# Kernel optimization log

Hardware: AMD Instinct MI355X
Metric: run time of the kernel (lower is better)

The kernel has to match this reference:

```python
import jax, jax.numpy as jnp
import numpy as np

B, S, DIM, H, FR = 2, 1568, 768, 12, 8  # S = FR * 196 spatial tokens, head_dim = 64


def setup_inputs() -> dict:
    key = jax.random.key(0)
    ks = jax.random.split(key, 8)
    s = 0.02
    return {
        "xq": jax.random.normal(ks[0], (B, S, DIM), jnp.float32),
        "xk": jax.random.normal(ks[1], (B, S, DIM), jnp.float32),
        "Wq": jax.random.normal(ks[2], (DIM, DIM), jnp.float32) * s,
        "Wkv": jax.random.normal(ks[3], (DIM, 2 * DIM), jnp.float32) * s,
        "Wpq": jax.random.normal(ks[4], (DIM, DIM), jnp.float32) * s,
        "Wpkv": jax.random.normal(ks[5], (DIM, 2 * DIM), jnp.float32) * s,
        "Wproj": jax.random.normal(ks[6], (DIM, DIM), jnp.float32) * s,
        "bproj": jnp.zeros((DIM,), jnp.float32),
        "num_frames": FR,
    }


def reference(xq, xk, Wq, Wkv, Wpq, Wpkv, Wproj, bproj, num_frames):
    b, s, dim = xq.shape
    f = num_frames
    n = xk.shape[1] // f          # spatial tokens per frame
    h = H
    d = dim // h
    scale = d ** -0.5

    # stage 1: space attention per frame
    q = (xq @ Wq).reshape(b, s, h, d).transpose(0, 2, 1, 3)            # b h s d
    k, v = jnp.split(xk @ Wkv, 2, axis=-1)
    k = k.reshape(b, f * n, h, d).transpose(0, 2, 1, 3)                # b h m d
    v = v.reshape(b, f * n, h, d).transpose(0, 2, 1, 3)                # b h m d
    qk = jnp.einsum('bhsd,bhmd->bhsm', q, k).reshape(b, h, s, f, n)
    attn = jax.nn.softmax(scale * qk, axis=-1)                         # b h s f n
    vf = v.reshape(b, h, f, n, d)
    x = jnp.einsum('bhsfn,bhfnd->bhsfd', attn, vf)                     # b h s f d
    x = x.transpose(0, 2, 3, 1, 4).reshape(b, s, f, dim)               # b s f (h d)

    # diagonal gather: trajectory token for its own frame
    xg = x.reshape(b, f, n, f, dim)
    x_diag = jnp.diagonal(xg, axis1=1, axis2=3)                        # b n dim f
    x_diag = x_diag.transpose(0, 3, 1, 2).reshape(b, s, dim)           # b (f n) dim

    # stage 2: temporal attention over frames
    q2 = (x_diag @ Wpq).reshape(b, s, h, d).transpose(0, 2, 1, 3) * scale  # b h s d
    k2, v2 = jnp.split(x @ Wpkv, 2, axis=-1)
    k2 = k2.reshape(b, s, f, h, d).transpose(0, 3, 1, 2, 4)            # b h s f d
    v2 = v2.reshape(b, s, f, h, d).transpose(0, 3, 1, 2, 4)
    attn2 = jax.nn.softmax(jnp.einsum('bhsd,bhsfd->bhsf', q2, k2), axis=-1)
    out = jnp.einsum('bhsf,bhsfd->bhsd', attn2, v2)                    # b h s d
    out = out.transpose(0, 2, 1, 3).reshape(b, s, dim) @ Wproj + bproj
    return (out, attn2)
```

## Files before the change

### kernel.cpp

```cpp
#include <hip/hip_runtime.h>

#define BDIM 2
#define SEQ  1568
#define DIM  768
#define NH   12
#define FR   8
#define NTOK 196
#define HD   64
#define MTOT (BDIM*SEQ)
#define M2   (MTOT*FR)

typedef __attribute__((ext_vector_type(8))) short s16x8;
typedef __attribute__((ext_vector_type(4))) float f32x4;
typedef __attribute__((ext_vector_type(16))) float f32x16;
typedef __attribute__((ext_vector_type(4))) int i32x4;

static __device__ __forceinline__ float bf2f(ushort u) {
  return __uint_as_float(((unsigned)u) << 16);
}
static __device__ __forceinline__ ushort f2bf(float f) {
  unsigned u = __float_as_uint(f);
  unsigned r = (u + 0x7fffu + ((u >> 16) & 1u)) >> 16;
  return (ushort)r;
}
static __device__ __forceinline__ f32x4 mfma16(s16x8 a, s16x8 b, f32x4 c) {
  return __builtin_amdgcn_mfma_f32_16x16x32_bf16(a, b, c, 0, 0, 0);
}
static __device__ __forceinline__ f32x16 mfma32(s16x8 a, s16x8 b, f32x16 c) {
  return __builtin_amdgcn_mfma_f32_32x32x16_bf16(a, b, c, 0, 0, 0);
}
static __device__ __forceinline__ int cvtpk(float lo, float hi) {
  int r;
  asm("v_cvt_pk_bf16_f32 %0, %1, %2" : "=v"(r) : "v"(lo), "v"(hi));
  return r;
}
static __device__ __forceinline__ void gload_lds16(const ushort* g, ushort* l) {
  __builtin_amdgcn_global_load_lds(
      (const __attribute__((address_space(1))) void*)g,
      (__attribute__((address_space(3))) void*)l, 16, 0, 0);
}

__global__ __launch_bounds__(256)
void cvt_all(const float* __restrict__ xq, const float* __restrict__ xk,
             ushort* __restrict__ xqbf, ushort* __restrict__ xkbf,
             const float* __restrict__ Wq, const float* __restrict__ Wkv,
             const float* __restrict__ Wpq, const float* __restrict__ Wproj,
             const float* __restrict__ Wpkv,
             ushort* __restrict__ WqT, ushort* __restrict__ WkvT,
             ushort* __restrict__ WpqT, ushort* __restrict__ WprT,
             ushort* __restrict__ Wpk_bf, ushort* __restrict__ Wpv_bf,
             int n4) {
  __shared__ float T[64][65];
  const int blk = blockIdx.x;
  const int tid = threadIdx.x;

  if (blk < 4704) {
    int i = blk*256 + tid;
    const float* src; ushort* dst; int j;
    if (i < n4)        { src = xq; dst = xqbf; j = i; }
    else               { src = xk; dst = xkbf; j = i - n4; }
    float4 v = ((const float4*)src)[j];
    ushort4 o; o.x = f2bf(v.x); o.y = f2bf(v.y); o.z = f2bf(v.z); o.w = f2bf(v.w);
    ((ushort4*)dst)[j] = o;
    return;
  }

  if (blk < 5856) {
    int idx = blk - 4704;
    const int wid = idx / 288; idx %= 288;
    const int ky = idx / 24;
    const int nx = idx % 24;
    const float* W; ushort* WT; int N;
    switch (wid) {
      case 0: W = Wq;    WT = WqT;   N = DIM;   break;
      case 1: W = Wkv;   WT = WkvT;  N = 2*DIM; break;
      case 2: W = Wpq;   WT = WpqT;  N = DIM;   break;
      default: W = Wproj; WT = WprT; N = DIM;   break;
    }
    if (nx >= N/64) return;
    #pragma unroll
    for (int it = 0; it < 4; it++) {
      int id2 = it*256 + tid;
      int r = id2 >> 4, c4 = (id2 & 15) << 2;
      float4 v = *(const float4*)&W[(size_t)(ky*64 + r)*N + nx*64 + c4];
      T[r][c4+0] = v.x; T[r][c4+1] = v.y; T[r][c4+2] = v.z; T[r][c4+3] = v.w;
    }
    __syncthreads();
    #pragma unroll
    for (int it = 0; it < 4; it++) {
      int id2 = it*256 + tid;
      int n = id2 >> 4, k4 = (id2 & 15) << 2;
      ushort4 o;
      o.x = f2bf(T[k4+0][n]); o.y = f2bf(T[k4+1][n]);
      o.z = f2bf(T[k4+2][n]); o.w = f2bf(T[k4+3][n]);
      *(ushort4*)&WT[(size_t)(nx*64 + n)*DIM + ky*64 + k4] = o;
    }
    return;
  }

  {
    int id2 = blk - 5856;
    int half = id2 / 576;
    int e = (id2 % 576)*256 + tid;
    int r = e / 192;
    int c4 = (e % 192) * 4;
    float4 v = *(const float4*)&Wpkv[(size_t)r*(2*DIM) + half*DIM + c4];
    ushort4 o; o.x = f2bf(v.x); o.y = f2bf(v.y); o.z = f2bf(v.z); o.w = f2bf(v.w);
    ushort* dst = half ? Wpv_bf : Wpk_bf;
    *(ushort4*)&dst[(size_t)r*DIM + c4] = o;
  }
}

__global__ __launch_bounds__(256)
void vtrans(const ushort* __restrict__ kvbf, ushort* __restrict__ Vt) {
  __shared__ ushort Vl[NTOK][72];
  const int x = blockIdx.x;
  const int h = x % NH, f = (x / NH) % FR, b = x / (NH*FR);
  const int tid = threadIdx.x;
  for (int idx = tid; idx < NTOK*16; idx += 256) {
    int n = idx >> 4, c4 = (idx & 15) << 2;
    const ushort* p = kvbf + (size_t)(b*SEQ + f*NTOK + n)*(2*DIM) + DIM + h*HD + c4;
    *(ushort4*)&Vl[n][c4] = *(const ushort4*)p;
  }
  __syncthreads();
  ushort* vb = Vt + (size_t)x * (HD*224);
  for (int idx = tid; idx < 64*56; idx += 256) {
    int d = idx / 56, n4 = (idx % 56) << 2;
    ushort4 o;
    o.x = (n4+0 < NTOK) ? Vl[n4+0][d] : (ushort)0;
    o.y = (n4+1 < NTOK) ? Vl[n4+1][d] : (ushort)0;
    o.z = (n4+2 < NTOK) ? Vl[n4+2][d] : (ushort)0;
    o.w = (n4+3 < NTOK) ? Vl[n4+3][d] : (ushort)0;
    *(ushort4*)&vb[(size_t)d*224 + n4] = o;
  }
}

__global__ __launch_bounds__(256)
void proj_pair(const ushort* __restrict__ xqbf, const ushort* __restrict__ xkbf,
               const ushort* __restrict__ WqT, const ushort* __restrict__ WkvT,
               ushort* __restrict__ qbf, ushort* __restrict__ kvbf)
{
  __shared__ ushort As[128][32];
  __shared__ ushort Bs[64][32];
  const int bx = blockIdx.x, by = blockIdx.y;
  const ushort* A; const ushort* Bt; ushort* C; int N, col0; float scale;
  if (bx < 12) { A = xqbf; Bt = WqT;  C = qbf;  N = DIM;   col0 = bx*64;      scale = 0.125f; }
  else         { A = xkbf; Bt = WkvT; C = kvbf; N = 2*DIM; col0 = (bx-12)*64; scale = 1.0f; }

  const int tid = threadIdx.x;
  const int w = tid >> 6, lane = tid & 63;
  const int lq = lane & 15, quad = lane >> 4;
  const int lrow = tid >> 2, lcol = (tid & 3) << 3;

  int ar0 = by*128 + lrow;       if (ar0 > MTOT-1) ar0 = MTOT-1;
  int ar1 = by*128 + 64 + lrow;  if (ar1 > MTOT-1) ar1 = MTOT-1;
  const size_t aoff0 = (size_t)ar0*DIM + lcol;
  const size_t aoff1 = (size_t)ar1*DIM + lcol;
  const size_t boff  = (size_t)(col0 + lrow)*DIM + lcol;

  f32x4 acc[2][4] = {};
  for (int k0 = 0; k0 < DIM; k0 += 32) {
    __syncthreads();
    gload_lds16(A  + aoff0 + k0, &As[w*16][0]);
    gload_lds16(A  + aoff1 + k0, &As[64 + w*16][0]);
    gload_lds16(Bt + boff  + k0, &Bs[w*16][0]);
    __syncthreads();
    s16x8 af[2], bw[4];
    #pragma unroll
    for (int i = 0; i < 2; i++) af[i] = *(const s16x8*)&As[w*32 + i*16 + lq][quad*8];
    #pragma unroll
    for (int j = 0; j < 4; j++) bw[j] = *(const s16x8*)&Bs[j*16 + lq][quad*8];
    #pragma unroll
    for (int i = 0; i < 2; i++)
      #pragma unroll
      for (int j = 0; j < 4; j++)
        acc[i][j] = mfma16(af[i], bw[j], acc[i][j]);
  }

  #pragma unroll
  for (int i = 0; i < 2; i++) {
    #pragma unroll
    for (int r = 0; r < 4; r++) {
      int row = by*128 + w*32 + i*16 + quad*4 + r;
      if (row < MTOT) {
        #pragma unroll
        for (int j = 0; j < 4; j++)
          C[(size_t)row*N + col0 + j*16 + lq] = f2bf(acc[i][j][r] * scale);
      }
    }
  }
}

template<bool BIAS, bool DIAG, bool BF16OUT>
__global__ __launch_bounds__(256)
void gemm64(const ushort* __restrict__ A, const ushort* __restrict__ Bt,
            void* __restrict__ Cv, const float* __restrict__ bias,
            int M, int N, float scale)
{
  __shared__ ushort As[128][32];
  __shared__ ushort Bs[64][32];
  const int bx = blockIdx.x, by = blockIdx.y;
  const int tid = threadIdx.x;
  const int w = tid >> 6, lane = tid & 63;
  const int lq = lane & 15, quad = lane >> 4;
  const int lrow = tid >> 2, lcol = (tid & 3) << 3;
  const int col0 = bx*64;

  int ar0 = by*128 + lrow;       if (ar0 > M-1) ar0 = M-1;
  int ar1 = by*128 + 64 + lrow;  if (ar1 > M-1) ar1 = M-1;
  size_t aoff0, aoff1;
  if (DIAG) {
    int f0 = (ar0 % SEQ) / NTOK, f1 = (ar1 % SEQ) / NTOK;
    aoff0 = ((size_t)ar0*FR + f0)*DIM + lcol;
    aoff1 = ((size_t)ar1*FR + f1)*DIM + lcol;
  } else {
    aoff0 = (size_t)ar0*DIM + lcol;
    aoff1 = (size_t)ar1*DIM + lcol;
  }
  const size_t boff = (size_t)(col0 + lrow)*DIM + lcol;

  f32x4 acc[2][4] = {};
  for (int k0 = 0; k0 < DIM; k0 += 32) {
    __syncthreads();
    gload_lds16(A  + aoff0 + k0, &As[w*16][0]);
    gload_lds16(A  + aoff1 + k0, &As[64 + w*16][0]);
    gload_lds16(Bt + boff  + k0, &Bs[w*16][0]);
    __syncthreads();
    s16x8 af[2], bw[4];
    #pragma unroll
    for (int i = 0; i < 2; i++) af[i] = *(const s16x8*)&As[w*32 + i*16 + lq][quad*8];
    #pragma unroll
    for (int j = 0; j < 4; j++) bw[j] = *(const s16x8*)&Bs[j*16 + lq][quad*8];
    #pragma unroll
    for (int i = 0; i < 2; i++)
      #pragma unroll
      for (int j = 0; j < 4; j++)
        acc[i][j] = mfma16(af[i], bw[j], acc[i][j]);
  }

  #pragma unroll
  for (int i = 0; i < 2; i++) {
    #pragma unroll
    for (int r = 0; r < 4; r++) {
      int row = by*128 + w*32 + i*16 + quad*4 + r;
      if (row < M) {
        #pragma unroll
        for (int j = 0; j < 4; j++) {
          int col = col0 + j*16 + lq;
          float v = acc[i][j][r] * scale;
          if (BIAS) v += bias[col];
          if (BF16OUT) ((ushort*)Cv)[(size_t)row*N + col] = f2bf(v);
          else         ((float*)Cv)[(size_t)row*N + col] = v;
        }
      }
    }
  }
}

__global__ __launch_bounds__(256)
void qwgemm(const ushort* __restrict__ q2bf, const ushort* __restrict__ Wpk,
            ushort* __restrict__ qw)
{
  __shared__ ushort As[128][32];
  __shared__ ushort Bs[64][32];
  const int bx = blockIdx.x, by = blockIdx.y;
  const int h = bx / 12, cb = bx % 12;
  const int tid = threadIdx.x;
  const int w = tid >> 6, lane = tid & 63;
  const int lq = lane & 15, quad = lane >> 4;
  const int lrow = tid >> 2, lcol = (tid & 3) << 3;

  int ar0 = by*128 + lrow;       if (ar0 > MTOT-1) ar0 = MTOT-1;
  int ar1 = by*128 + 64 + lrow;  if (ar1 > MTOT-1) ar1 = MTOT-1;
  const size_t aoff0 = (size_t)ar0*DIM + h*HD + lcol;
  const size_t aoff1 = (size_t)ar1*DIM + h*HD + lcol;
  const size_t boff  = (size_t)(cb*64 + lrow)*DIM + h*HD + lcol;

  f32x4 acc[2][4] = {};
  #pragma unroll
  for (int k0 = 0; k0 < 64; k0 += 32) {
    __syncthreads();
    gload_lds16(q2bf + aoff0 + k0, &As[w*16][0]);
    gload_lds16(q2bf + aoff1 + k0, &As[64 + w*16][0]);
    gload_lds16(Wpk  + boff  + k0, &Bs[w*16][0]);
    __syncthreads();
    s16x8 af[2], bw[4];
    #pragma unroll
    for (int i = 0; i < 2; i++) af[i] = *(const s16x8*)&As[w*32 + i*16 + lq][quad*8];
    #pragma unroll
    for (int jj = 0; jj < 4; jj++) bw[jj] = *(const s16x8*)&Bs[jj*16 + lq][quad*8];
    #pragma unroll
    for (int i = 0; i < 2; i++)
      #pragma unroll
      for (int jj = 0; jj < 4; jj++)
        acc[i][jj] = mfma16(af[i], bw[jj], acc[i][jj]);
  }

  #pragma unroll
  for (int i = 0; i < 2; i++) {
    #pragma unroll
    for (int r = 0; r < 4; r++) {
      int row = by*128 + w*32 + i*16 + quad*4 + r;
      if (row < MTOT) {
        #pragma unroll
        for (int jj = 0; jj < 4; jj++) {
          int cl = cb*64 + jj*16 + lq;
          qw[(size_t)row*(NH*DIM) + h*DIM + cl] = f2bf(acc[i][r == r ? i*0 + jj : jj][r]);
        }
      }
    }
  }
}

__global__ __launch_bounds__(256)
void logits_sa(const ushort* __restrict__ qw, const ushort* __restrict__ x,
               float* __restrict__ attn2, ushort* __restrict__ xa)
{
  __shared__ ushort xs[4*8*792];
  __shared__ ushort qws[4*12*792];
  __shared__ float  a_s[4][NH][FR];
  const int tid = threadIdx.x;
  const int t0 = blockIdx.x * 4;

  #pragma unroll
  for (int r = 0; r < 12; ++r) {
    int id = r*256 + tid;
    int tf = id / 96, v8 = id % 96;
    int ch = v8 >> 5, cc = v8 & 31;
    s16x8 v = *(const s16x8*)(x + ((size_t)(t0 + (tf >> 3))*FR + (tf & 7))*DIM + v8*8);
    *(s16x8*)&xs[tf*792 + ch*264 + cc*8] = v;
  }
  #pragma unroll
  for (int r = 0; r < 18; ++r) {
    int id = r*256 + tid;
    int th = id / 96, v8 = id % 96;
    int ch = v8 >> 5, cc = v8 & 31;
    s16x8 v = *(const s16x8*)(qw + (size_t)(t0 + th/12)*(NH*DIM) + (th%12)*DIM + v8*8);
    *(s16x8*)&qws[th*792 + ch*264 + cc*8] = v;
  }
  __syncthreads();

  const int w = tid >> 6, lane = tid & 63;
  const int lq = lane & 15, quad = lane >> 4;
  const int fr = lq & 7;
  const int hc = (lq < 12) ? lq : 0;
  f32x4 acc = {};
  #pragma unroll
  for (int ks = 0; ks < 24; ++ks) {
    int ch = ks >> 3, cc = (ks & 7) * 32;
    s16x8 a = *(const s16x8*)&xs[(w*8 + fr)*792 + ch*264 + cc + quad*8];
    s16x8 b = *(const s16x8*)&qws[(w*12 + hc)*792 + ch*264 + cc + quad*8];
    acc = mfma16(a, b, acc);
  }

  float m4 = fmaxf(fmaxf(acc[0], acc[1]), fmaxf(acc[2], acc[3]));
  float M = fmaxf(m4, __shfl_xor(m4, 16));
  float e0 = __expf(acc[0]-M), e1 = __expf(acc[1]-M);
  float e2 = __expf(acc[2]-M), e3 = __expf(acc[3]-M);
  float s4 = (e0+e1)+(e2+e3);
  float S = s4 + __shfl_xor(s4, 16);
  float inv = 1.0f / S;
  if (quad < 2 && lq < 12) {
    int gt = t0 + w;
    int b = gt / SEQ, sI = gt % SEQ;
    float4 av; av.x = e0*inv; av.y = e1*inv; av.z = e2*inv; av.w = e3*inv;
    *(float4*)(attn2 + ((size_t)(b*NH + hc)*SEQ + sI)*FR + quad*4) = av;
    a_s[w][hc][quad*4+0] = av.x; a_s[w][hc][quad*4+1] = av.y;
    a_s[w][hc][quad*4+2] = av.z; a_s[w][hc][quad*4+3] = av.w;
  }
  __syncthreads();

  #pragma unroll
  for (int it = 0; it < 2; ++it) {
    int id = it*256 + tid;
    if (id < 384) {
      int tt = id / 96, v8 = id % 96;
      int ch = v8 >> 5, cc = v8 & 31;
      int h = v8 >> 3;
      float av[8] = {};
      #pragma unroll
      for (int f = 0; f < FR; ++f) {
        float a = a_s[tt][h][f];
        s16x8 xv = *(const s16x8*)&xs[(tt*8 + f)*792 + ch*264 + cc*8];
        #pragma unroll
        for (int e = 0; e < 8; ++e) av[e] += a * bf2f((ushort)xv[e]);
      }
      ushort4 o0, o1;
      o0.x = f2bf(av[0]); o0.y = f2bf(av[1]); o0.z = f2bf(av[2]); o0.w = f2bf(av[3]);
      o1.x = f2bf(av[4]); o1.y = f2bf(av[5]); o1.z = f2bf(av[6]); o1.w = f2bf(av[7]);
      ushort* op = xa + (size_t)(t0 + tt)*DIM + v8*8;
      *(ushort4*)op = o0; *(ushort4*)(op + 4) = o1;
    }
  }
}

__global__ __launch_bounds__(256)
void stage1_mfma(const ushort* __restrict__ qbf, const ushort* __restrict__ kvbf,
                 const ushort* __restrict__ Vt, ushort* __restrict__ x)
{
  __shared__ ushort sh[208*64];

  const int bh = blockIdx.x;
  const int f  = blockIdx.y;
  const int qt = blockIdx.z;
  const int b = bh / NH, h = bh % NH;
  const int tid = threadIdx.x;
  const int w = tid >> 6, lane = tid & 63;
  const int l31 = lane & 31, hl = lane >> 5;

  const ushort* kbase = kvbf + ((size_t)b*SEQ + f*NTOK)*(2*DIM) + h*HD;
  #pragma unroll
  for (int p = 0; p < 6; ++p) {
    const int c = w*6 + p;
    const int row = c*8 + (lane >> 3);
    const ushort* src = kbase + (size_t)row*(2*DIM)
                      + (((lane & 7) ^ (lane >> 3)) << 3);
    gload_lds16(src, &sh[c*512]);
  }
  {
    const int row = 192 + (tid >> 4);
    const int c4  = (tid & 15) << 2;
    ushort4 v; v.x = 0; v.y = 0; v.z = 0; v.w = 0;
    if (row < NTOK)
      v = *(const ushort4*)(kbase + (size_t)row*(2*DIM) + c4);
    *(ushort4*)&sh[row*64 + ((((c4 >> 3) ^ (row & 7)) << 3) | (c4 & 7))] = v;
  }

  int qrow = qt*128 + w*32 + l31; if (qrow > SEQ-1) qrow = SEQ-1;
  const ushort* qp = qbf + ((size_t)b*SEQ + qrow)*DIM + h*HD + hl*8;
  const s16x8 bq0 = *(const s16x8*)(qp);
  const s16x8 bq1 = *(const s16x8*)(qp + 16);
  const s16x8 bq2 = *(const s16x8*)(qp + 32);
  const s16x8 bq3 = *(const s16x8*)(qp + 48);

  __syncthreads();

  f32x16 acc[7];
  {
    f32x16 z = {};
    #pragma unroll
    for (int nt = 0; nt < 7; ++nt) acc[nt] = z;
  }
  const int sx = l31 & 7;
  #pragma unroll
  for (int nt = 0; nt < 7; ++nt) {
    const int rl = (nt == 6) ? (l31 & 15) : l31;
    const int rbase = (nt*32 + rl)*64;
    acc[nt] = mfma32(*(const s16x8*)&sh[rbase + (((0 + hl) ^ sx) << 3)], bq0, acc[nt]);
    acc[nt] = mfma32(*(const s16x8*)&sh[rbase + (((2 + hl) ^ sx) << 3)], bq1, acc[nt]);
    acc[nt] = mfma32(*(const s16x8*)&sh[rbase + (((4 + hl) ^ sx) << 3)], bq2, acc[nt]);
    acc[nt] = mfma32(*(const s16x8*)&sh[rbase + (((6 + hl) ^ sx) << 3)], bq3, acc[nt]);
  }

  __syncthreads();

  float s0 = 0.f, s1 = 0.f, s2 = 0.f, s3 = 0.f;
  #pragma unroll
  for (int nt = 0; nt < 7; ++nt) {
    #pragma unroll
    for (int g = 0; g < 16; ++g) {
      float e;
      if (nt == 6) {
        if (g < 4) { e = __expf(acc[6][g]); if (hl) e = 0.f; }
        else e = 0.f;
      } else {
        e = __expf(acc[nt][g]);
      }
      acc[nt][g] = e;
      if ((g & 3) == 0) s0 += e; else if ((g & 3) == 1) s1 += e;
      else if ((g & 3) == 2) s2 += e; else s3 += e;
    }
  }
  float sum = (s0 + s1) + (s2 + s3);
  sum += __shfl_xor(sum, 32);
  const float sinv = 1.0f / sum;

  f32x16 o0, o1;
  { f32x16 z = {}; o0 = z; o1 = z; }
  const ushort* vb = Vt + ((size_t)((b*FR + f)*NH + h)) * (HD*224);
  const ushort* vr0 = vb + (size_t)l31*224 + hl*8;
  const ushort* vr1 = vr0 + 32*224;
  #pragma unroll
  for (int nt = 0; nt < 7; ++nt) {
    #pragma unroll
    for (int kh = 0; kh < 2; ++kh) {
      int w0 = cvtpk(acc[nt][8*kh+0], acc[nt][8*kh+1]);
      int w1 = cvtpk(acc[nt][8*kh+2], acc[nt][8*kh+3]);
      int w2 = cvtpk(acc[nt][8*kh+4], acc[nt][8*kh+5]);
      int w3 = cvtpk(acc[nt][8*kh+6], acc[nt][8*kh+7]);
      asm("v_permlane32_swap_b32 %0, %1" : "+v"(w0), "+v"(w2));
      asm("v_permlane32_swap_b32 %0, %1" : "+v"(w1), "+v"(w3));
      union { i32x4 i; s16x8 s; } u;
      u.i.x = w0; u.i.y = w1; u.i.z = w2; u.i.w = w3;
      const int ks = nt*2 + kh;
      const s16x8 va0 = *(const s16x8*)(vr0 + ks*16);
      const s16x8 va1 = *(const s16x8*)(vr1 + ks*16);
      o0 = mfma32(va0, u.s, o0);
      o1 = mfma32(va1, u.s, o1);
    }
  }

  ushort* XT = sh + w*2048;
  #pragma unroll
  for (int dt = 0; dt < 2; ++dt) {
    #pragma unroll
    for (int c = 0; c < 4; ++c) {
      #pragma unroll
      for (int rp = 0; rp < 2; ++rp) {
        const float lo = (dt ? o1[4*c + 2*rp]     : o0[4*c + 2*rp])     * sinv;
        const float hi = (dt ? o1[4*c + 2*rp + 1] : o0[4*c + 2*rp + 1]) * sinv;
        const int word = cvtpk(lo, hi);
        const int d = dt*32 + 8*c + 4*hl + 2*rp;
        *(uint*)&XT[l31*64 + (((d >> 3) ^ (l31 & 7)) << 3) + (d & 7)] = (uint)word;
      }
    }
  }
  #pragma unroll
  for (int it = 0; it < 4; ++it) {
    const int q = it*8 + (lane >> 3);
    const int g = lane & 7;
    s16x8 xv = *(const s16x8*)&XT[q*64 + ((g ^ (q & 7)) << 3)];
    const int s = qt*128 + w*32 + q;
    if (s < SEQ) {
      ushort* xp = x + (((size_t)b*SEQ + s)*FR + f)*DIM + h*HD + g*8;
      *(s16x8*)xp = xv;
    }
  }
}

extern "C" void kernel_launch(void* const* d_in, const int* in_sizes, int n_in,
                              void* d_out, int out_size, void* d_ws, size_t ws_size,
                              hipStream_t stream) {
  const float* xq    = (const float*)d_in[0];
  const float* xk    = (const float*)d_in[1];
  const float* Wq    = (const float*)d_in[2];
  const float* Wkv   = (const float*)d_in[3];
  const float* Wpq   = (const float*)d_in[4];
  const float* Wpkv  = (const float*)d_in[5];
  const float* Wproj = (const float*)d_in[6];
  const float* bproj = (const float*)d_in[7];

  float* out   = (float*)d_out;
  float* attn2 = out + (size_t)MTOT*DIM;

  ushort* ws     = (ushort*)d_ws;
  ushort* xbf    = ws;
  ushort* kvbf   = xbf + (size_t)MTOT*FR*DIM;
  ushort* q2bf   = kvbf;
  ushort* qbf    = kvbf + (size_t)MTOT*2*DIM;
  ushort* xqbf   = qbf + (size_t)MTOT*DIM;
  ushort* xkbf   = xqbf + (size_t)MTOT*DIM;
  ushort* Vt     = xqbf;
  ushort* xa     = xkbf;
  ushort* WqT    = xkbf + (size_t)MTOT*DIM;
  ushort* WkvT   = WqT  + (size_t)DIM*DIM;
  ushort* WpqT   = WkvT + (size_t)2*DIM*DIM;
  ushort* WprT   = WpqT + (size_t)DIM*DIM;
  ushort* Wpk_bf = WprT + (size_t)DIM*DIM;
  ushort* Wpv_bf = Wpk_bf + (size_t)DIM*DIM;
  ushort* WcombT = Wpv_bf + (size_t)DIM*DIM;
  ushort* qw     = WcombT + (size_t)DIM*DIM;

  dim3 blk(256);
  const int n4 = MTOT*DIM/4;

  cvt_all<<<dim3(4704 + 1152 + 1152), blk, 0, stream>>>(
      xq, xk, xqbf, xkbf, Wq, Wkv, Wpq, Wproj, Wpkv,
      WqT, WkvT, WpqT, WprT, Wpk_bf, Wpv_bf, n4);

  gemm64<false,false,true><<<dim3(12, 6), blk, 0, stream>>>(
      WprT, Wpv_bf, WcombT, nullptr, DIM, DIM, 1.0f);

  proj_pair<<<dim3(36, (MTOT+127)/128), blk, 0, stream>>>(
      xqbf, xkbf, WqT, WkvT, qbf, kvbf);
  vtrans<<<dim3(BDIM*FR*NH), blk, 0, stream>>>(kvbf, Vt);
  stage1_mfma<<<dim3(BDIM*NH, FR, (SEQ+127)/128), blk, 0, stream>>>(qbf, kvbf, Vt, xbf);

  gemm64<false,true,true><<<dim3(12, (MTOT+127)/128), blk, 0, stream>>>(
      xbf, WpqT, q2bf, nullptr, MTOT, DIM, 0.125f);

  qwgemm<<<dim3(144, 25), blk, 0, stream>>>(q2bf, Wpk_bf, qw);
  logits_sa<<<dim3(MTOT/4), blk, 0, stream>>>(qw, xbf, attn2, xa);

  gemm64<true,false,false><<<dim3(12, (MTOT+127)/128), blk, 0, stream>>>(
      xa, WcombT, out, bproj, MTOT, DIM, 1.0f);
}
```

Measured before the change: 245.9 us.

## Fuse diagonal q2 projection GEMM with per-head q·Wpk GEMM

Merges the q2 = x_diag·Wpq GEMM and the per-head q2·Wpk GEMM into one kernel. Each block computes a 128x64 per-head q2 tile in shared memory, then loops over 12 column tiles to produce qw. This removes one launch and the q2 round trip through global memory, but shrinks the grid from 144x25 to 12x25 blocks, so fewer blocks are resident and each does more serial work.

```diff
diff --git a/kernel.cpp b/kernel.cpp
--- a/kernel.cpp
+++ b/kernel.cpp
@@ -258,13 +258,13 @@
 }
 
 __global__ __launch_bounds__(256)
-void qwgemm(const ushort* __restrict__ q2bf, const ushort* __restrict__ Wpk,
-            ushort* __restrict__ qw)
+void q2qw(const ushort* __restrict__ x, const ushort* __restrict__ WpqT,
+          const ushort* __restrict__ Wpk, ushort* __restrict__ qw)
 {
   __shared__ ushort As[128][32];
   __shared__ ushort Bs[64][32];
-  const int bx = blockIdx.x, by = blockIdx.y;
-  const int h = bx / 12, cb = bx % 12;
+  __shared__ ushort q2s[128][72];
+  const int h = blockIdx.x, by = blockIdx.y;
   const int tid = threadIdx.x;
   const int w = tid >> 6, lane = tid & 63;
   const int lq = lane & 15, quad = lane >> 4;
@@ -272,40 +272,68 @@
 
   int ar0 = by*128 + lrow;       if (ar0 > MTOT-1) ar0 = MTOT-1;
   int ar1 = by*128 + 64 + lrow;  if (ar1 > MTOT-1) ar1 = MTOT-1;
-  const size_t aoff0 = (size_t)ar0*DIM + h*HD + lcol;
-  const size_t aoff1 = (size_t)ar1*DIM + h*HD + lcol;
-  const size_t boff  = (size_t)(cb*64 + lrow)*DIM + h*HD + lcol;
+  const int f0 = (ar0 % SEQ) / NTOK, f1 = (ar1 % SEQ) / NTOK;
+  const size_t aoff0 = ((size_t)ar0*FR + f0)*DIM + lcol;
+  const size_t aoff1 = ((size_t)ar1*FR + f1)*DIM + lcol;
+  const size_t boff  = (size_t)(h*64 + lrow)*DIM + lcol;
 
   f32x4 acc[2][4] = {};
-  #pragma unroll
-  for (int k0 = 0; k0 < 64; k0 += 32) {
+  for (int k0 = 0; k0 < DIM; k0 += 32) {
     __syncthreads();
-    gload_lds16(q2bf + aoff0 + k0, &As[w*16][0]);
-    gload_lds16(q2bf + aoff1 + k0, &As[64 + w*16][0]);
-    gload_lds16(Wpk  + boff  + k0, &Bs[w*16][0]);
+    gload_lds16(x    + aoff0 + k0, &As[w*16][0]);
+    gload_lds16(x    + aoff1 + k0, &As[64 + w*16][0]);
+    gload_lds16(WpqT + boff  + k0, &Bs[w*16][0]);
     __syncthreads();
     s16x8 af[2], bw[4];
     #pragma unroll
     for (int i = 0; i < 2; i++) af[i] = *(const s16x8*)&As[w*32 + i*16 + lq][quad*8];
     #pragma unroll
-    for (int jj = 0; jj < 4; jj++) bw[jj] = *(const s16x8*)&Bs[jj*16 + lq][quad*8];
+    for (int j = 0; j < 4; j++) bw[j] = *(const s16x8*)&Bs[j*16 + lq][quad*8];
     #pragma unroll
     for (int i = 0; i < 2; i++)
       #pragma unroll
-      for (int jj = 0; jj < 4; jj++)
-        acc[i][jj] = mfma16(af[i], bw[jj], acc[i][jj]);
-  }
-
-  #pragma unroll
-  for (int i = 0; i < 2; i++) {
+      for (int j = 0; j < 4; j++)
+        acc[i][j] = mfma16(af[i], bw[j], acc[i][j]);
+  }
+
+  #pragma unroll
+  for (int i = 0; i < 2; i++)
     #pragma unroll
     for (int r = 0; r < 4; r++) {
-      int row = by*128 + w*32 + i*16 + quad*4 + r;
-      if (row < MTOT) {
+      int row = w*32 + i*16 + quad*4 + r;
+      #pragma unroll
+      for (int j = 0; j < 4; j++)
+        q2s[row][j*16 + lq] = f2bf(acc[i][j][r] * 0.125f);
+    }
+
+  for (int ct = 0; ct < 12; ++ct) {
+    f32x4 acc2[2][4] = {};
+    #pragma unroll
+    for (int k0 = 0; k0 < 64; k0 += 32) {
+      __syncthreads();
+      gload_lds16(Wpk + (size_t)(ct*64 + lrow)*DIM + h*HD + k0 + lcol, &Bs[w*16][0]);
+      __syncthreads();
+      s16x8 af[2], bw[4];
+      #pragma unroll
+      for (int i = 0; i < 2; i++)
+        af[i] = *(const s16x8*)&q2s[w*32 + i*16 + lq][k0 + quad*8];
+      #pragma unroll
+      for (int j = 0; j < 4; j++) bw[j] = *(const s16x8*)&Bs[j*16 + lq][quad*8];
+      #pragma unroll
+      for (int i = 0; i < 2; i++)
         #pragma unroll
-        for (int jj = 0; jj < 4; jj++) {
-          int cl = cb*64 + jj*16 + lq;
-          qw[(size_t)row*(NH*DIM) + h*DIM + cl] = f2bf(acc[i][r == r ? i*0 + jj : jj][r]);
+        for (int j = 0; j < 4; j++)
+          acc2[i][j] = mfma16(af[i], bw[j], acc2[i][j]);
+    }
+    #pragma unroll
+    for (int i = 0; i < 2; i++) {
+      #pragma unroll
+      for (int r = 0; r < 4; r++) {
+        int row = by*128 + w*32 + i*16 + quad*4 + r;
+        if (row < MTOT) {
+          #pragma unroll
+          for (int j = 0; j < 4; j++)
+            qw[(size_t)row*(NH*DIM) + h*DIM + ct*64 + j*16 + lq] = f2bf(acc2[i][j][r]);
         }
       }
     }
@@ -546,7 +574,6 @@
   ushort* ws     = (ushort*)d_ws;
   ushort* xbf    = ws;
   ushort* kvbf   = xbf + (size_t)MTOT*FR*DIM;
-  ushort* q2bf   = kvbf;
   ushort* qbf    = kvbf + (size_t)MTOT*2*DIM;
   ushort* xqbf   = qbf + (size_t)MTOT*DIM;
   ushort* xkbf   = xqbf + (size_t)MTOT*DIM;
@@ -576,10 +603,8 @@
   vtrans<<<dim3(BDIM*FR*NH), blk, 0, stream>>>(kvbf, Vt);
   stage1_mfma<<<dim3(BDIM*NH, FR, (SEQ+127)/128), blk, 0, stream>>>(qbf, kvbf, Vt, xbf);
 
-  gemm64<false,true,true><<<dim3(12, (MTOT+127)/128), blk, 0, stream>>>(
-      xbf, WpqT, q2bf, nullptr, MTOT, DIM, 0.125f);
-
-  qwgemm<<<dim3(144, 25), blk, 0, stream>>>(q2bf, Wpk_bf, qw);
+  q2qw<<<dim3(12, 25), blk, 0, stream>>>(xbf, WpqT, Wpk_bf, qw);
+
   logits_sa<<<dim3(MTOT/4), blk, 0, stream>>>(qw, xbf, attn2, xa);
 
   gemm64<true,false,false><<<dim3(12, (MTOT+127)/128), blk, 0, stream>>>(
```

Result: no change. 243.9 us (-0.8%).
